# Kernel tuning notes

Hardware: AMD Instinct MI355X
Metric: run time of the kernel (lower is better)

The kernel has to match this reference:

```python
import jax, jax.numpy as jnp
import numpy as np
import math

FRACTION = 1.0 / math.e  # GOLDEN_ZONE_CENTER


def setup_inputs() -> dict:
    key = jax.random.key(0)
    x = jax.random.normal(key, (4, 4096, 2048), dtype=jnp.float32)
    return {"x": x}


def reference(x) -> jnp.ndarray:
    # Training-mode forward of BoltzmannGateSTE: keep only top-k (k = n/e)
    # activations by global magnitude, zero the rest.
    flat = jnp.abs(x).reshape(-1)
    n = flat.shape[0]
    k = max(1, int(n * FRACTION))  # static python int -> jit-friendly
    if k >= n:
        return x
    topk_vals, _ = jax.lax.top_k(flat, k)
    threshold = topk_vals[-1]  # k-th largest magnitude
    mask = (jnp.abs(x) >= threshold).astype(x.dtype)
    return x * mask
```

## Files before the change

kernel.cpp:

```cpp
#include <hip/hip_runtime.h>
#include <stdint.h>


#define SEL_T 1024

constexpr int H_BLOCKS = 512;
constexpr int H_THREADS = 1024;
constexpr int NBIN1   = 4096;
constexpr int NFINE   = 1 << 19;
constexpr int NCOARSE = 512;

__global__ __launch_bounds__(H_THREADS)
void hist_pass1(const uint4* __restrict__ x, long long n4, unsigned* __restrict__ hists)
{
    __shared__ unsigned h[NBIN1];
    for (int i = threadIdx.x; i < NBIN1; i += H_THREADS) h[i] = 0u;
    __syncthreads();
    long long stride = (long long)gridDim.x * H_THREADS;
    for (long long i = (long long)blockIdx.x * H_THREADS + threadIdx.x; i < n4; i += stride) {
        uint4 v = x[i];
        atomicAdd(&h[(v.x & 0x7FFFFFFFu) >> 19], 1u);
        atomicAdd(&h[(v.y & 0x7FFFFFFFu) >> 19], 1u);
        atomicAdd(&h[(v.z & 0x7FFFFFFFu) >> 19], 1u);
        atomicAdd(&h[(v.w & 0x7FFFFFFFu) >> 19], 1u);
    }
    __syncthreads();
    unsigned* out = hists + (size_t)blockIdx.x * NBIN1;
    for (int i = threadIdx.x; i < NBIN1; i += H_THREADS) out[i] = h[i];
}

__global__ void hist_reduce(const unsigned* __restrict__ hists, unsigned* __restrict__ histA,
                            int nblocks)
{
    int bin = blockIdx.x * blockDim.x + threadIdx.x;
    if (bin >= NBIN1) return;
    unsigned s = 0;
    for (int b = 0; b < nblocks; ++b) s += hists[(size_t)b * NBIN1 + bin];
    histA[bin] = s;
}

__device__ void select_desc(const unsigned* __restrict__ hist, int nbins,
                            unsigned k, unsigned* s_scan, int* s_res)
{
    int tid = threadIdx.x;
    if (tid == 0) { s_res[0] = -1; s_res[1] = 0; }
    __syncthreads();
    unsigned running = 0;
    for (int top = nbins; top > 0; top -= SEL_T) {
        int bin = top - 1 - tid;
        unsigned v = (bin >= 0) ? hist[bin] : 0u;
        s_scan[tid] = v;
        __syncthreads();
        for (int off = 1; off < SEL_T; off <<= 1) {
            unsigned add = (tid >= off) ? s_scan[tid - off] : 0u;
            __syncthreads();
            s_scan[tid] += add;
            __syncthreads();
        }
        unsigned p     = s_scan[tid];
        unsigned pprev = (tid > 0) ? s_scan[tid - 1] : 0u;
        unsigned total = s_scan[SEL_T - 1];
        __syncthreads();
        if (running + total >= k) {
            if (bin >= 0 && running + p >= k && running + pprev < k) {
                s_res[0] = bin;
                s_res[1] = (int)(k - running - pprev);
            }
            __syncthreads();
            return;
        }
        running += total;
    }
    if (tid == 0 && s_res[0] < 0) { s_res[0] = 0; s_res[1] = 1; }
    __syncthreads();
}

__global__ __launch_bounds__(SEL_T)
void select1_kernel(const unsigned* __restrict__ histA, unsigned* __restrict__ state, unsigned k)
{
    __shared__ unsigned s_scan[SEL_T];
    __shared__ int s_res[2];
    select_desc(histA, NBIN1, k, s_scan, s_res);
    if (threadIdx.x == 0) { state[0] = (unsigned)s_res[0]; state[1] = (unsigned)s_res[1]; }
}

__global__ __launch_bounds__(H_THREADS)
void hist_pass2(const uint4* __restrict__ x, long long n4, const unsigned* __restrict__ state,
                unsigned* __restrict__ fineB, unsigned* __restrict__ coarseB)
{
    __shared__ unsigned hc[NCOARSE];
    for (int i = threadIdx.x; i < NCOARSE; i += H_THREADS) hc[i] = 0u;
    __syncthreads();
    unsigned pref = state[0];
    long long stride = (long long)gridDim.x * H_THREADS;
    for (long long i = (long long)blockIdx.x * H_THREADS + threadIdx.x; i < n4; i += stride) {
        uint4 v = x[i];
        unsigned u;
        u = v.x & 0x7FFFFFFFu;
        if ((u >> 19) == pref) { atomicAdd(&fineB[u & (NFINE - 1)], 1u); atomicAdd(&hc[(u & (NFINE - 1)) >> 10], 1u); }
        u = v.y & 0x7FFFFFFFu;
        if ((u >> 19) == pref) { atomicAdd(&fineB[u & (NFINE - 1)], 1u); atomicAdd(&hc[(u & (NFINE - 1)) >> 10], 1u); }
        u = v.z & 0x7FFFFFFFu;
        if ((u >> 19) == pref) { atomicAdd(&fineB[u & (NFINE - 1)], 1u); atomicAdd(&hc[(u & (NFINE - 1)) >> 10], 1u); }
        u = v.w & 0x7FFFFFFFu;
        if ((u >> 19) == pref) { atomicAdd(&fineB[u & (NFINE - 1)], 1u); atomicAdd(&hc[(u & (NFINE - 1)) >> 10], 1u); }
    }
    __syncthreads();
    for (int i = threadIdx.x; i < NCOARSE; i += H_THREADS)
        if (hc[i]) atomicAdd(&coarseB[i], hc[i]);
}

__global__ __launch_bounds__(SEL_T)
void select2_kernel(const unsigned* __restrict__ fineB, const unsigned* __restrict__ coarseB,
                    unsigned* __restrict__ state)
{
    __shared__ unsigned s_scan[SEL_T];
    __shared__ int s_res[2];
    unsigned pref = state[0];
    unsigned k    = state[1];
    select_desc(coarseB, NCOARSE, k, s_scan, s_res);
    int c       = s_res[0];
    unsigned k1 = (unsigned)s_res[1];
    __syncthreads();
    select_desc(fineB + (size_t)c * 1024, 1024, k1, s_scan, s_res);
    int f = s_res[0];
    if (threadIdx.x == 0)
        state[2] = (pref << 19) | ((unsigned)c << 10) | (unsigned)f;
}

__global__ __launch_bounds__(256)
void mask_kernel(const uint4* __restrict__ x, uint4* __restrict__ out, long long n4,
                 const unsigned* __restrict__ state)
{
    unsigned t = state[2];
    long long stride = (long long)gridDim.x * 256;
    for (long long i = (long long)blockIdx.x * 256 + threadIdx.x; i < n4; i += stride) {
        uint4 v = x[i];
        uint4 r;
        r.x = ((v.x & 0x7FFFFFFFu) >= t) ? v.x : 0u;
        r.y = ((v.y & 0x7FFFFFFFu) >= t) ? v.y : 0u;
        r.z = ((v.z & 0x7FFFFFFFu) >= t) ? v.z : 0u;
        r.w = ((v.w & 0x7FFFFFFFu) >= t) ? v.w : 0u;
        out[i] = r;
    }
}

extern "C" void kernel_launch(void* const* d_in, const int* in_sizes, int n_in,
                              void* d_out, int out_size, void* d_ws, size_t ws_size,
                              hipStream_t stream)
{
    long long n  = (long long)in_sizes[0];
    if (n <= 0) return;
    long long n4 = n >> 2;

    const double FRACTION = 1.0 / 2.718281828459045;
    long long k = (long long)((double)n * FRACTION);
    if (k < 1) k = 1;

    size_t off_hists  = 0;
    size_t off_histA  = off_hists  + (size_t)H_BLOCKS * NBIN1 * 4;
    size_t off_fineB  = off_histA  + (size_t)NBIN1 * 4;
    size_t off_coarse = off_fineB  + (size_t)NFINE * 4;
    size_t off_state  = off_coarse + (size_t)NCOARSE * 4;
    size_t need       = off_state + 64;

    uint8_t* base;
    unsigned* state;
    if (ws_size >= need) {
        base  = (uint8_t*)d_ws;
        state = (unsigned*)(base + off_state);
    } else {
        base  = (uint8_t*)d_out;
        state = (unsigned*)d_ws;
    }
    unsigned* hists   = (unsigned*)(base + off_hists);
    unsigned* histA   = (unsigned*)(base + off_histA);
    unsigned* fineB   = (unsigned*)(base + off_fineB);
    unsigned* coarseB = (unsigned*)(base + off_coarse);

    hipMemsetAsync(fineB, 0, ((size_t)NFINE + NCOARSE) * 4, stream);
    hipMemsetAsync(state, 0, 16, stream);

    const uint4* x = (const uint4*)d_in[0];

    hist_pass1 <<<H_BLOCKS, H_THREADS, 0, stream>>>(x, n4, hists);
    hist_reduce<<<(NBIN1 + 255) / 256, 256, 0, stream>>>(hists, histA, H_BLOCKS);
    select1_kernel<<<1, SEL_T, 0, stream>>>(histA, state, (unsigned)k);
    hist_pass2 <<<H_BLOCKS, H_THREADS, 0, stream>>>(x, n4, state, fineB, coarseB);
    select2_kernel<<<1, SEL_T, 0, stream>>>(fineB, coarseB, state);
    mask_kernel<<<2048, 256, 0, stream>>>(x, (uint4*)d_out, n4, state);
}
```

Measured before the change: 365.5 us.

## Add single-pass candidate-band selection with fallback to multi-pass radix histogram

Adds a fast path that reads the input once. It writes every element above a fixed magnitude cutoff straight to the output, and collects elements inside a narrow band [0.88, 0.92) into per-block candidate buffers along with a coarse histogram. The exact threshold is then found from the candidates alone, and the fixup writes back the band elements that pass. This replaces three full passes over the input with one. If the band does not contain the threshold or a candidate buffer overflows, a flag sends execution to the original multi-pass path. The band bounds assume the activations roughly follow a unit normal. The fast path also needs a much larger workspace.

```diff
diff --git a/kernel.cpp b/kernel.cpp
--- a/kernel.cpp
+++ b/kernel.cpp
@@ -1,42 +1,73 @@
 #include <hip/hip_runtime.h>
 #include <stdint.h>
+#include <string.h>
 
 
 #define SEL_T 1024
 
-constexpr int H_BLOCKS = 512;
+constexpr int H_BLOCKS  = 512;
 constexpr int H_THREADS = 1024;
-constexpr int NBIN1   = 4096;
-constexpr int NFINE   = 1 << 19;
-constexpr int NCOARSE = 512;
+constexpr int NBIN1     = 4096;
+constexpr int NFINE     = 1 << 19;
+constexpr int NCOARSE   = 512;
+constexpr int CAP       = 8192;
+
+#define S_PREF 0
+#define S_K1   1
+#define S_T    2
+#define S_FLAG 3
+#define S_CHI  4
+
+__device__ __forceinline__ bool gate_skip(const unsigned* state, int gate) {
+    if (gate == 0) return false;
+    unsigned fl = state[S_FLAG];
+    return (gate == 1) ? (fl == 0u) : (fl != 0u);
+}
 
 __global__ __launch_bounds__(H_THREADS)
-void hist_pass1(const uint4* __restrict__ x, long long n4, unsigned* __restrict__ hists)
-{
-    __shared__ unsigned h[NBIN1];
-    for (int i = threadIdx.x; i < NBIN1; i += H_THREADS) h[i] = 0u;
-    __syncthreads();
+void pass_partition(const uint4* __restrict__ x, long long n4,
+                    unsigned lo, unsigned hi,
+                    uint4* __restrict__ out, uint2* __restrict__ cand,
+                    unsigned* __restrict__ bcnt, unsigned* __restrict__ chist,
+                    unsigned* __restrict__ state, int cap)
+{
+    __shared__ unsigned h12[NBIN1];
+    __shared__ unsigned s_cnt;
+    for (int i = threadIdx.x; i < NBIN1; i += H_THREADS) h12[i] = 0u;
+    if (threadIdx.x == 0) s_cnt = 0u;
+    __syncthreads();
+
+    uint2* mycand = cand + (size_t)blockIdx.x * cap;
+    unsigned chi = 0;
     long long stride = (long long)gridDim.x * H_THREADS;
     for (long long i = (long long)blockIdx.x * H_THREADS + threadIdx.x; i < n4; i += stride) {
         uint4 v = x[i];
-        atomicAdd(&h[(v.x & 0x7FFFFFFFu) >> 19], 1u);
-        atomicAdd(&h[(v.y & 0x7FFFFFFFu) >> 19], 1u);
-        atomicAdd(&h[(v.z & 0x7FFFFFFFu) >> 19], 1u);
-        atomicAdd(&h[(v.w & 0x7FFFFFFFu) >> 19], 1u);
-    }
-    __syncthreads();
-    unsigned* out = hists + (size_t)blockIdx.x * NBIN1;
-    for (int i = threadIdx.x; i < NBIN1; i += H_THREADS) out[i] = h[i];
-}
-
-__global__ void hist_reduce(const unsigned* __restrict__ hists, unsigned* __restrict__ histA,
-                            int nblocks)
-{
-    int bin = blockIdx.x * blockDim.x + threadIdx.x;
-    if (bin >= NBIN1) return;
-    unsigned s = 0;
-    for (int b = 0; b < nblocks; ++b) s += hists[(size_t)b * NBIN1 + bin];
-    histA[bin] = s;
+        uint4 r;
+        unsigned idx0 = (unsigned)((unsigned long long)i << 2);
+#define DO_COMP(c, off)                                                          \
+        { unsigned u = v.c & 0x7FFFFFFFu;                                        \
+          bool kp = (u >= hi);                                                   \
+          chi += kp ? 1u : 0u;                                                   \
+          r.c = kp ? v.c : 0u;                                                   \
+          if (u >= lo && !kp) {                                                  \
+              atomicAdd(&h12[u >> 19], 1u);                                      \
+              unsigned s = atomicAdd(&s_cnt, 1u);                                \
+              if ((int)s < cap) mycand[s] = make_uint2(v.c, idx0 + off);         \
+          } }
+        DO_COMP(x, 0) DO_COMP(y, 1) DO_COMP(z, 2) DO_COMP(w, 3)
+#undef DO_COMP
+        out[i] = r;
+    }
+
+    for (int m = 32; m; m >>= 1) chi += __shfl_xor(chi, m, 64);
+    __syncthreads();
+    for (int i = threadIdx.x; i < NBIN1; i += H_THREADS)
+        if (h12[i]) atomicAdd(&chist[i], h12[i]);
+    if ((threadIdx.x & 63) == 0) atomicAdd(&state[S_CHI], chi);
+    if (threadIdx.x == 0) {
+        bcnt[blockIdx.x] = s_cnt;
+        if ((int)s_cnt > cap) atomicOr(&state[S_FLAG], 1u);
+    }
 }
 
 __device__ void select_desc(const unsigned* __restrict__ hist, int nbins,
@@ -71,68 +102,162 @@
         }
         running += total;
     }
-    if (tid == 0 && s_res[0] < 0) { s_res[0] = 0; s_res[1] = 1; }
     __syncthreads();
 }
 
 __global__ __launch_bounds__(SEL_T)
-void select1_kernel(const unsigned* __restrict__ histA, unsigned* __restrict__ state, unsigned k)
-{
+void cand_select12(const unsigned* __restrict__ chist, unsigned* __restrict__ state,
+                   unsigned k)
+{
+    if (state[S_FLAG]) return;
+    __shared__ unsigned s_scan[SEL_T];
+    __shared__ int s_res[2];
+    unsigned chi = state[S_CHI];
+    if (chi >= k) { if (threadIdx.x == 0) state[S_FLAG] = 1u; return; }
+    select_desc(chist, NBIN1, k - chi, s_scan, s_res);
+    if (threadIdx.x == 0) {
+        if (s_res[0] < 0) state[S_FLAG] = 1u;
+        else { state[S_PREF] = (unsigned)s_res[0]; state[S_K1] = (unsigned)s_res[1]; }
+    }
+}
+
+__global__ __launch_bounds__(256)
+void cand_hist_fine(const uint2* __restrict__ cand, const unsigned* __restrict__ bcnt,
+                    const unsigned* __restrict__ state,
+                    unsigned* __restrict__ fineB, unsigned* __restrict__ coarseB, int cap)
+{
+    if (state[S_FLAG]) return;
+    __shared__ unsigned hc[NCOARSE];
+    for (int i = threadIdx.x; i < NCOARSE; i += 256) hc[i] = 0u;
+    __syncthreads();
+    unsigned pref = state[S_PREF];
+    unsigned cnt  = bcnt[blockIdx.x];
+    if (cnt > (unsigned)cap) cnt = (unsigned)cap;
+    const uint2* my = cand + (size_t)blockIdx.x * cap;
+    for (unsigned j = threadIdx.x; j < cnt; j += 256) {
+        unsigned u = my[j].x & 0x7FFFFFFFu;
+        if ((u >> 19) == pref) {
+            unsigned f = u & (NFINE - 1);
+            atomicAdd(&fineB[f], 1u);
+            atomicAdd(&hc[f >> 10], 1u);
+        }
+    }
+    __syncthreads();
+    for (int i = threadIdx.x; i < NCOARSE; i += 256)
+        if (hc[i]) atomicAdd(&coarseB[i], hc[i]);
+}
+
+__global__ __launch_bounds__(SEL_T)
+void select2_kernel(const unsigned* __restrict__ fineB, const unsigned* __restrict__ coarseB,
+                    unsigned* __restrict__ state, int gate)
+{
+    if (gate_skip(state, gate)) return;
+    __shared__ unsigned s_scan[SEL_T];
+    __shared__ int s_res[2];
+    unsigned pref = state[S_PREF];
+    unsigned k    = state[S_K1];
+    select_desc(coarseB, NCOARSE, k, s_scan, s_res);
+    int c       = (s_res[0] < 0) ? 0 : s_res[0];
+    unsigned k1 = (s_res[0] < 0) ? 1u : (unsigned)s_res[1];
+    __syncthreads();
+    select_desc(fineB + (size_t)c * 1024, 1024, k1, s_scan, s_res);
+    int f = (s_res[0] < 0) ? 0 : s_res[0];
+    if (threadIdx.x == 0)
+        state[S_T] = (pref << 19) | ((unsigned)c << 10) | (unsigned)f;
+}
+
+__global__ __launch_bounds__(256)
+void cand_fixup(const uint2* __restrict__ cand, const unsigned* __restrict__ bcnt,
+                const unsigned* __restrict__ state, float* __restrict__ out, int cap)
+{
+    if (state[S_FLAG]) return;
+    unsigned T   = state[S_T];
+    unsigned cnt = bcnt[blockIdx.x];
+    if (cnt > (unsigned)cap) cnt = (unsigned)cap;
+    const uint2* my = cand + (size_t)blockIdx.x * cap;
+    for (unsigned j = threadIdx.x; j < cnt; j += 256) {
+        uint2 e = my[j];
+        if ((e.x & 0x7FFFFFFFu) >= T) out[e.y] = __uint_as_float(e.x);
+    }
+}
+
+__global__ __launch_bounds__(H_THREADS)
+void hist_pass1(const uint4* __restrict__ x, long long n4, unsigned* __restrict__ hists,
+                const unsigned* __restrict__ state, int gate)
+{
+    if (gate_skip(state, gate)) return;
+    __shared__ unsigned h[NBIN1];
+    for (int i = threadIdx.x; i < NBIN1; i += H_THREADS) h[i] = 0u;
+    __syncthreads();
+    long long stride = (long long)gridDim.x * H_THREADS;
+    for (long long i = (long long)blockIdx.x * H_THREADS + threadIdx.x; i < n4; i += stride) {
+        uint4 v = x[i];
+        atomicAdd(&h[(v.x & 0x7FFFFFFFu) >> 19], 1u);
+        atomicAdd(&h[(v.y & 0x7FFFFFFFu) >> 19], 1u);
+        atomicAdd(&h[(v.z & 0x7FFFFFFFu) >> 19], 1u);
+        atomicAdd(&h[(v.w & 0x7FFFFFFFu) >> 19], 1u);
+    }
+    __syncthreads();
+    unsigned* o = hists + (size_t)blockIdx.x * NBIN1;
+    for (int i = threadIdx.x; i < NBIN1; i += H_THREADS) o[i] = h[i];
+}
+
+__global__ void hist_reduce(const unsigned* __restrict__ hists, unsigned* __restrict__ histA,
+                            int nblocks, const unsigned* __restrict__ state, int gate)
+{
+    if (gate_skip(state, gate)) return;
+    int bin = blockIdx.x * blockDim.x + threadIdx.x;
+    if (bin >= NBIN1) return;
+    unsigned s = 0;
+    for (int b = 0; b < nblocks; ++b) s += hists[(size_t)b * NBIN1 + bin];
+    histA[bin] = s;
+}
+
+__global__ __launch_bounds__(SEL_T)
+void select1_kernel(const unsigned* __restrict__ histA, unsigned* __restrict__ state,
+                    unsigned k, int gate)
+{
+    if (gate_skip(state, gate)) return;
     __shared__ unsigned s_scan[SEL_T];
     __shared__ int s_res[2];
     select_desc(histA, NBIN1, k, s_scan, s_res);
-    if (threadIdx.x == 0) { state[0] = (unsigned)s_res[0]; state[1] = (unsigned)s_res[1]; }
+    if (threadIdx.x == 0) {
+        state[S_PREF] = (s_res[0] < 0) ? 0u : (unsigned)s_res[0];
+        state[S_K1]   = (s_res[0] < 0) ? 1u : (unsigned)s_res[1];
+    }
 }
 
 __global__ __launch_bounds__(H_THREADS)
 void hist_pass2(const uint4* __restrict__ x, long long n4, const unsigned* __restrict__ state,
-                unsigned* __restrict__ fineB, unsigned* __restrict__ coarseB)
-{
+                unsigned* __restrict__ fineB, unsigned* __restrict__ coarseB, int gate)
+{
+    if (gate_skip(state, gate)) return;
     __shared__ unsigned hc[NCOARSE];
     for (int i = threadIdx.x; i < NCOARSE; i += H_THREADS) hc[i] = 0u;
     __syncthreads();
-    unsigned pref = state[0];
+    unsigned pref = state[S_PREF];
     long long stride = (long long)gridDim.x * H_THREADS;
     for (long long i = (long long)blockIdx.x * H_THREADS + threadIdx.x; i < n4; i += stride) {
         uint4 v = x[i];
         unsigned u;
-        u = v.x & 0x7FFFFFFFu;
-        if ((u >> 19) == pref) { atomicAdd(&fineB[u & (NFINE - 1)], 1u); atomicAdd(&hc[(u & (NFINE - 1)) >> 10], 1u); }
-        u = v.y & 0x7FFFFFFFu;
-        if ((u >> 19) == pref) { atomicAdd(&fineB[u & (NFINE - 1)], 1u); atomicAdd(&hc[(u & (NFINE - 1)) >> 10], 1u); }
-        u = v.z & 0x7FFFFFFFu;
-        if ((u >> 19) == pref) { atomicAdd(&fineB[u & (NFINE - 1)], 1u); atomicAdd(&hc[(u & (NFINE - 1)) >> 10], 1u); }
-        u = v.w & 0x7FFFFFFFu;
-        if ((u >> 19) == pref) { atomicAdd(&fineB[u & (NFINE - 1)], 1u); atomicAdd(&hc[(u & (NFINE - 1)) >> 10], 1u); }
+#define DO_C(c) u = v.c & 0x7FFFFFFFu;                                           \
+        if ((u >> 19) == pref) {                                                 \
+            atomicAdd(&fineB[u & (NFINE - 1)], 1u);                              \
+            atomicAdd(&hc[(u & (NFINE - 1)) >> 10], 1u); }
+        DO_C(x) DO_C(y) DO_C(z) DO_C(w)
+#undef DO_C
     }
     __syncthreads();
     for (int i = threadIdx.x; i < NCOARSE; i += H_THREADS)
         if (hc[i]) atomicAdd(&coarseB[i], hc[i]);
 }
 
-__global__ __launch_bounds__(SEL_T)
-void select2_kernel(const unsigned* __restrict__ fineB, const unsigned* __restrict__ coarseB,
-                    unsigned* __restrict__ state)
-{
-    __shared__ unsigned s_scan[SEL_T];
-    __shared__ int s_res[2];
-    unsigned pref = state[0];
-    unsigned k    = state[1];
-    select_desc(coarseB, NCOARSE, k, s_scan, s_res);
-    int c       = s_res[0];
-    unsigned k1 = (unsigned)s_res[1];
-    __syncthreads();
-    select_desc(fineB + (size_t)c * 1024, 1024, k1, s_scan, s_res);
-    int f = s_res[0];
-    if (threadIdx.x == 0)
-        state[2] = (pref << 19) | ((unsigned)c << 10) | (unsigned)f;
-}
-
 __global__ __launch_bounds__(256)
 void mask_kernel(const uint4* __restrict__ x, uint4* __restrict__ out, long long n4,
-                 const unsigned* __restrict__ state)
-{
-    unsigned t = state[2];
+                 const unsigned* __restrict__ state, int gate)
+{
+    if (gate_skip(state, gate)) return;
+    unsigned t = state[S_T];
     long long stride = (long long)gridDim.x * 256;
     for (long long i = (long long)blockIdx.x * 256 + threadIdx.x; i < n4; i += stride) {
         uint4 v = x[i];
@@ -149,7 +274,7 @@
                               void* d_out, int out_size, void* d_ws, size_t ws_size,
                               hipStream_t stream)
 {
-    long long n  = (long long)in_sizes[0];
+    long long n = (long long)in_sizes[0];
     if (n <= 0) return;
     long long n4 = n >> 2;
 
@@ -157,36 +282,60 @@
     long long k = (long long)((double)n * FRACTION);
     if (k < 1) k = 1;
 
-    size_t off_hists  = 0;
-    size_t off_histA  = off_hists  + (size_t)H_BLOCKS * NBIN1 * 4;
-    size_t off_fineB  = off_histA  + (size_t)NBIN1 * 4;
-    size_t off_coarse = off_fineB  + (size_t)NFINE * 4;
-    size_t off_state  = off_coarse + (size_t)NCOARSE * 4;
-    size_t need       = off_state + 64;
-
-    uint8_t* base;
-    unsigned* state;
-    if (ws_size >= need) {
-        base  = (uint8_t*)d_ws;
-        state = (unsigned*)(base + off_state);
+    unsigned lo, hi;
+    { float f = 0.88f; memcpy(&lo, &f, 4); lo &= 0x7FFFFFFFu; }
+    { float f = 0.92f; memcpy(&hi, &f, 4); hi &= 0x7FFFFFFFu; }
+
+    const size_t off_histA  = 0;
+    const size_t off_chist  = off_histA  + (size_t)NBIN1 * 4;
+    const size_t off_fineB  = off_chist  + (size_t)NBIN1 * 4;
+    const size_t off_coarse = off_fineB  + (size_t)NFINE * 4;
+    const size_t off_bcnt   = off_coarse + (size_t)NCOARSE * 4;
+    const size_t off_hists  = off_bcnt   + (size_t)H_BLOCKS * 4;
+    const size_t off_cand   = off_hists  + (size_t)H_BLOCKS * NBIN1 * 4;
+    const size_t cand_bytes = (size_t)H_BLOCKS * CAP * 8;
+    const size_t need_fast  = 64 + off_cand + cand_bytes;
+    const size_t need_ws    = 64 + off_cand;
+
+    unsigned* state = (unsigned*)d_ws;
+    uint8_t*  bb;
+    bool fast;
+    if (ws_size >= need_fast)      { bb = (uint8_t*)d_ws + 64; fast = true;  }
+    else if (ws_size >= need_ws)   { bb = (uint8_t*)d_ws + 64; fast = false; }
+    else                           { bb = (uint8_t*)d_out;     fast = false; }
+
+    unsigned* histA   = (unsigned*)(bb + off_histA);
+    unsigned* chist   = (unsigned*)(bb + off_chist);
+    unsigned* fineB   = (unsigned*)(bb + off_fineB);
+    unsigned* coarseB = (unsigned*)(bb + off_coarse);
+    unsigned* bcnt    = (unsigned*)(bb + off_bcnt);
+    unsigned* hists   = (unsigned*)(bb + off_hists);
+    uint2*    cand    = (uint2*)   (bb + off_cand);
+
+    hipMemsetAsync(bb, 0, off_bcnt, stream);
+    hipMemsetAsync(state, 0, 64, stream);
+
+    const uint4* x = (const uint4*)d_in[0];
+
+    if (fast) {
+        pass_partition<<<H_BLOCKS, H_THREADS, 0, stream>>>(x, n4, lo, hi, (uint4*)d_out,
+                                                           cand, bcnt, chist, state, CAP);
+        cand_select12 <<<1, SEL_T, 0, stream>>>(chist, state, (unsigned)k);
+        cand_hist_fine<<<H_BLOCKS, 256, 0, stream>>>(cand, bcnt, state, fineB, coarseB, CAP);
+        select2_kernel<<<1, SEL_T, 0, stream>>>(fineB, coarseB, state, 2);
+        cand_fixup    <<<H_BLOCKS, 256, 0, stream>>>(cand, bcnt, state, (float*)d_out, CAP);
+        hist_pass1    <<<H_BLOCKS, H_THREADS, 0, stream>>>(x, n4, hists, state, 1);
+        hist_reduce   <<<(NBIN1 + 255) / 256, 256, 0, stream>>>(hists, histA, H_BLOCKS, state, 1);
+        select1_kernel<<<1, SEL_T, 0, stream>>>(histA, state, (unsigned)k, 1);
+        hist_pass2    <<<H_BLOCKS, H_THREADS, 0, stream>>>(x, n4, state, fineB, coarseB, 1);
+        select2_kernel<<<1, SEL_T, 0, stream>>>(fineB, coarseB, state, 1);
+        mask_kernel   <<<2048, 256, 0, stream>>>(x, (uint4*)d_out, n4, state, 1);
     } else {
-        base  = (uint8_t*)d_out;
-        state = (unsigned*)d_ws;
-    }
-    unsigned* hists   = (unsigned*)(base + off_hists);
-    unsigned* histA   = (unsigned*)(base + off_histA);
-    unsigned* fineB   = (unsigned*)(base + off_fineB);
-    unsigned* coarseB = (unsigned*)(base + off_coarse);
-
-    hipMemsetAsync(fineB, 0, ((size_t)NFINE + NCOARSE) * 4, stream);
-    hipMemsetAsync(state, 0, 16, stream);
-
-    const uint4* x = (const uint4*)d_in[0];
-
-    hist_pass1 <<<H_BLOCKS, H_THREADS, 0, stream>>>(x, n4, hists);
-    hist_reduce<<<(NBIN1 + 255) / 256, 256, 0, stream>>>(hists, histA, H_BLOCKS);
-    select1_kernel<<<1, SEL_T, 0, stream>>>(histA, state, (unsigned)k);
-    hist_pass2 <<<H_BLOCKS, H_THREADS, 0, stream>>>(x, n4, state, fineB, coarseB);
-    select2_kernel<<<1, SEL_T, 0, stream>>>(fineB, coarseB, state);
-    mask_kernel<<<2048, 256, 0, stream>>>(x, (uint4*)d_out, n4, state);
-}
+        hist_pass1    <<<H_BLOCKS, H_THREADS, 0, stream>>>(x, n4, hists, state, 0);
+        hist_reduce   <<<(NBIN1 + 255) / 256, 256, 0, stream>>>(hists, histA, H_BLOCKS, state, 0);
+        select1_kernel<<<1, SEL_T, 0, stream>>>(histA, state, (unsigned)k, 0);
+        hist_pass2    <<<H_BLOCKS, H_THREADS, 0, stream>>>(x, n4, state, fineB, coarseB, 0);
+        select2_kernel<<<1, SEL_T, 0, stream>>>(fineB, coarseB, state, 0);
+        mask_kernel   <<<2048, 256, 0, stream>>>(x, (uint4*)d_out, n4, state, 0);
+    }
+}
```

After: 388.1 us. 6.2% more time.
